# Kernel tuning notes

Hardware: AMD Instinct MI355X
Metric: run time of the kernel (lower is better)

## Reference

```python
import jax, jax.numpy as jnp
import numpy as np
from jax import lax

P = 3            # patch_size
H = W = 32       # spatial size forced by reshape to (32,32)
RATES = (1, 2, 4, 8)
DN = ('NCHW', 'OIHW', 'NCHW')


def setup_inputs() -> dict:
    key = jax.random.key(0)
    k0, k1, k2, k3 = jax.random.split(key, 4)
    foreground = jax.random.normal(k0, (8, 256, H, W), jnp.float32)
    background = jax.random.normal(k1, (8, 256, H, W), jnp.float32)
    mask = (jax.random.uniform(k2, (1, 1, H, W)) < 0.5).astype(jnp.float32)  # binary hole mask
    conv_w = jax.random.normal(k3, (4, 64, 256, 3, 3), jnp.float32) * 0.02
    conv_b = jnp.zeros((4, 64), jnp.float32)
    return {"foreground": foreground, "mask": mask, "background": background,
            "conv_w": conv_w, "conv_b": conv_b}


def _extract_patches(x):
    # x: [C, H+2, W+2] (padded) -> [H*W, C, 3, 3], patch index = h*W + w (torch unfold order)
    C = x.shape[0]
    cols = jnp.stack([x[:, i:i + H, j:j + W] for i in range(P) for j in range(P)], axis=0)  # [9,C,H,W]
    return cols.reshape(P, P, C, H, W).transpose(3, 4, 2, 0, 1).reshape(H * W, C, P, P)


def _forward(foreground, mask, background, conv_w, conv_b):
    bg = background * (1.0 - mask)
    bg_p = jnp.pad(bg, ((0, 0), (0, 0), (1, 1), (1, 1)))
    # per-sample patch kernels, L2-normalized (cosine similarity)
    kernels = jax.vmap(_extract_patches)(bg_p) + 1e-7          # [bz, L=1024, C, 3, 3]
    norm = jnp.sqrt(jnp.sum(kernels ** 2, axis=(2, 3, 4), keepdims=True))
    kernels = kernels / norm

    def corr(fm, kern):  # fm [C,H,W], kern [L,C,3,3] -> [L,H,W]
        return lax.conv_general_dilated(fm[None], kern, (1, 1), 'SAME', dimension_numbers=DN)[0]

    scores = jax.vmap(corr)(foreground, kernels)               # [bz, L, H, W]
    # propagation: depthwise 3x3 ones conv (groups=L, padding=1) == windowed sum
    scores = lax.reduce_window(scores, jnp.float32(0), lax.add,
                               (1, 1, 3, 3), (1, 1, 1, 1), 'SAME')
    attn = jax.nn.softmax(scores, axis=1)                      # softmax over the L patch axis

    def tconv(a, kern):
        # conv_transpose2d(a, kern[in=L,out=C], padding=1) == conv2d with spatially
        # flipped kernels and in/out swapped, padding = 3-1-1 = 1 (SAME)
        wct = jnp.flip(kern, axis=(2, 3)).transpose(1, 0, 2, 3)  # [C, L, 3, 3]
        return lax.conv_general_dilated(a[None], wct, (1, 1), 'SAME', dimension_numbers=DN)[0]

    recovered = jax.vmap(tconv)(attn, kernels)                 # [bz, C, H, W]
    recovered = recovered * mask / (P * P)
    final = recovered + foreground * (1.0 - mask)

    outs = []
    for g in range(4):  # 4 fused dilated conv branches (structurally distinct weights)
        r = RATES[g]
        o = lax.conv_general_dilated(final, conv_w[g], (1, 1), [(r, r), (r, r)],
                                     rhs_dilation=(r, r), dimension_numbers=DN)
        outs.append(jax.nn.relu(o + conv_b[g][None, :, None, None]))
    return jnp.concatenate(outs, axis=1)                       # [bz, 256, H, W]


def reference(foreground, mask, background, conv_w, conv_b):
    return _forward(foreground, mask, background, conv_w, conv_b)
```

## Files before the change

kernel.cpp:

```cpp
#include <hip/hip_runtime.h>

typedef __attribute__((ext_vector_type(8))) short short8;
typedef __attribute__((ext_vector_type(4))) float f32x4;
typedef __attribute__((ext_vector_type(4))) unsigned int uint4v;

#define HW 32
#define L 1024
#define C_IN 256
#define BATCH 8
#define NQ 1156

static __device__ __forceinline__ unsigned short f2bf(float f){
  unsigned int u = __float_as_uint(f);
  unsigned int r = (u + 0x7FFFu + ((u >> 16) & 1u)) >> 16;
  return (unsigned short)r;
}
static __device__ __forceinline__ float bf2f(unsigned short h){
  return __uint_as_float(((unsigned int)h) << 16);
}

#define GLDS16(g, l) __builtin_amdgcn_global_load_lds(                          \
    (const __attribute__((address_space(1))) void*)(g),                         \
    (__attribute__((address_space(3))) void*)(l), 16, 0, 0)

__global__ __launch_bounds__(256) void fused_prep(const float* __restrict__ fg,
                                                  const float* __restrict__ bgd,
                                                  const float* __restrict__ mask,
                                                  unsigned short* __restrict__ fgT,
                                                  unsigned short* __restrict__ mbgT,
                                                  unsigned short* __restrict__ mbgS,
                                                  float* __restrict__ psum,
                                                  const float* __restrict__ conv_w,
                                                  unsigned short* __restrict__ Wr,
                                                  unsigned short* __restrict__ zpage){
  __shared__ float T[64][65];
  int blk = blockIdx.x;
  if (blk >= 512){
    if (blk == 512) zpage[threadIdx.x] = 0;
    int idx = (blk - 512) * 256 + threadIdx.x;
    int c = idx & 255;
    int rest = idx >> 8;
    int n = rest & 63;
    int sg = rest >> 6;
    int s = sg % 9, g = sg / 9;
    Wr[idx] = f2bf(conv_w[(((size_t)(g * 64 + n)) * C_IN + c) * 9 + s]);
    return;
  }
  const int NP = BATCH * L;
  int bx = blk & 15, cb = (blk >> 4) & 3, b = blk >> 6;
  int p0 = bx * 64, c0 = cb * 64;
  int tid = threadIdx.x;
  int rr = tid >> 4, px = (tid & 15) * 4;
  int cx = tid & 15, ppb = tid >> 4;
  const float* F = fg  + ((size_t)b * C_IN + c0) * L + p0;
  const float* G = bgd + ((size_t)b * C_IN + c0) * L + p0;

  #pragma unroll
  for (int it = 0; it < 4; it++){
    int cc = it * 16 + rr;
    float4 v = *(const float4*)(F + (size_t)cc * L + px);
    T[cc][px] = v.x; T[cc][px + 1] = v.y; T[cc][px + 2] = v.z; T[cc][px + 3] = v.w;
  }
  __syncthreads();
  #pragma unroll
  for (int it = 0; it < 4; it++){
    int pp = it * 16 + ppb;
    float t0 = T[cx * 4][pp], t1 = T[cx * 4 + 1][pp], t2 = T[cx * 4 + 2][pp], t3 = T[cx * 4 + 3][pp];
    ushort4 o; o.x = f2bf(t0); o.y = f2bf(t1); o.z = f2bf(t2); o.w = f2bf(t3);
    *(ushort4*)&fgT[(size_t)(b * L + p0 + pp) * C_IN + c0 + cx * 4] = o;
    float s = t0 + t1 + t2 + t3;
    #pragma unroll
    for (int off = 8; off; off >>= 1) s += __shfl_xor(s, off, 16);
    if (cx == 0) psum[(size_t)(cb * 3 + 0) * NP + b * L + p0 + pp] = s;
  }
  __syncthreads();

  float4 mv = *(const float4*)(mask + p0 + px);
  mv.x = 1.f - mv.x; mv.y = 1.f - mv.y; mv.z = 1.f - mv.z; mv.w = 1.f - mv.w;
  #pragma unroll
  for (int it = 0; it < 4; it++){
    int cc = it * 16 + rr;
    float4 v = *(const float4*)(G + (size_t)cc * L + px);
    v.x *= mv.x; v.y *= mv.y; v.z *= mv.z; v.w *= mv.w;
    T[cc][px] = v.x; T[cc][px + 1] = v.y; T[cc][px + 2] = v.z; T[cc][px + 3] = v.w;
    ushort4 o; o.x = f2bf(v.x); o.y = f2bf(v.y); o.z = f2bf(v.z); o.w = f2bf(v.w);
    *(ushort4*)&mbgS[((size_t)b * C_IN + c0 + cc) * L + p0 + px] = o;
  }
  __syncthreads();
  #pragma unroll
  for (int it = 0; it < 4; it++){
    int pp = it * 16 + ppb;
    float t0 = T[cx * 4][pp], t1 = T[cx * 4 + 1][pp], t2 = T[cx * 4 + 2][pp], t3 = T[cx * 4 + 3][pp];
    ushort4 o; o.x = f2bf(t0); o.y = f2bf(t1); o.z = f2bf(t2); o.w = f2bf(t3);
    *(ushort4*)&mbgT[(size_t)(b * L + p0 + pp) * C_IN + c0 + cx * 4] = o;
    float s1 = t0 + t1 + t2 + t3;
    float s2 = t0 * t0 + t1 * t1 + t2 * t2 + t3 * t3;
    #pragma unroll
    for (int off = 8; off; off >>= 1){
      s1 += __shfl_xor(s1, off, 16);
      s2 += __shfl_xor(s2, off, 16);
    }
    if (cx == 0){
      psum[(size_t)(cb * 3 + 1) * NP + b * L + p0 + pp] = s1;
      psum[(size_t)(cb * 3 + 2) * NP + b * L + p0 + pp] = s2;
    }
  }
}

__global__ __launch_bounds__(256) void gemm_d_rn(const unsigned short* __restrict__ fgT,
                                                 const unsigned short* __restrict__ mbgT,
                                                 unsigned short* __restrict__ D,
                                                 const float* __restrict__ psum,
                                                 float* __restrict__ rn,
                                                 float* __restrict__ eps){
  __shared__ unsigned short As[64][256];
  __shared__ unsigned short Bs[64][256];
  int bid = blockIdx.x;
  if (bid >= 2048){
    int idx = (bid - 2048) * 256 + threadIdx.x;
    int b = idx >> 10, l = idx & 1023;
    int ly = l >> 5, lx = l & 31;
    const int NP = BATCH * L;
    float n2 = 2.304e-11f;
    #pragma unroll
    for (int s = 0; s < 9; s++){
      int y = ly + s / 3 - 1, x = lx + s % 3 - 1;
      if ((unsigned)y < HW && (unsigned)x < HW){
        int q = b * L + y * HW + x;
        float s1 = 0.f, s2 = 0.f;
        #pragma unroll
        for (int k = 0; k < 4; k++){
          s1 += psum[(size_t)(k * 3 + 1) * NP + q];
          s2 += psum[(size_t)(k * 3 + 2) * NP + q];
        }
        n2 += s2 + 2e-7f * s1;
      }
    }
    rn[idx] = 1.f / sqrtf(n2);
    float ev = 0.f;
    const int tw[5] = {1, 2, 3, 2, 1};
    #pragma unroll
    for (int oy = -2; oy <= 2; oy++)
      #pragma unroll
      for (int ox = -2; ox <= 2; ox++){
        int y = ly + oy, x = lx + ox;
        if ((unsigned)y < HW && (unsigned)x < HW){
          int q = b * L + y * HW + x;
          float s0 = 0.f;
          #pragma unroll
          for (int k = 0; k < 4; k++) s0 += psum[(size_t)(k * 3 + 0) * NP + q];
          ev += (float)(tw[oy + 2] * tw[ox + 2]) * s0;
        }
      }
    eps[idx] = 1e-7f * ev;
    return;
  }
  int b = bid & 7, r = bid >> 3;
  int by = r >> 4, bx = r & 15;
  const unsigned short* Ab = fgT  + ((size_t)b * L + by * 64) * C_IN;
  const unsigned short* Bb = mbgT + ((size_t)b * L + bx * 64) * C_IN;
  int tid = threadIdx.x, lane = tid & 63, wv = tid >> 6;
  int row_off = lane >> 5, slot = lane & 31;
  int q = slot >> 3, sl = slot & 7;
  #pragma unroll
  for (int i = 0; i < 8; i++){
    int rr = wv * 16 + i * 2 + row_off;
    int srcs = q * 8 + (sl ^ (rr & 7));
    GLDS16(Ab + (size_t)rr * C_IN + srcs * 8, &As[wv * 16 + i * 2][0]);
    GLDS16(Bb + (size_t)rr * C_IN + srcs * 8, &Bs[wv * 16 + i * 2][0]);
  }
  __syncthreads();
  int wm = (wv & 1) * 32, wn = (wv >> 1) * 32;
  int rsel = lane & 15, sx = lane >> 4;
  f32x4 acc[2][2] = {};
  #pragma unroll
  for (int st = 0; st < 8; st++){
    int gs = st * 4 + sx, qq = gs >> 3, ss = gs & 7;
    short8 af[2], bf[2];
    #pragma unroll
    for (int i = 0; i < 2; i++){
      int ra = wm + i * 16 + rsel;
      af[i] = *(const short8*)&As[ra][(qq * 8 + (ss ^ (ra & 7))) * 8];
      int rb = wn + i * 16 + rsel;
      bf[i] = *(const short8*)&Bs[rb][(qq * 8 + (ss ^ (rb & 7))) * 8];
    }
    #pragma unroll
    for (int i = 0; i < 2; i++)
      #pragma unroll
      for (int j = 0; j < 2; j++)
        acc[i][j] = __builtin_amdgcn_mfma_f32_16x16x32_bf16(af[i], bf[j], acc[i][j], 0, 0, 0);
  }
  unsigned short* Db = D + ((size_t)b << 20);
  int rowb = (lane >> 4) * 4, col = lane & 15;
  #pragma unroll
  for (int i = 0; i < 2; i++)
    #pragma unroll
    for (int j = 0; j < 2; j++)
      #pragma unroll
      for (int r2 = 0; r2 < 4; r2++)
        Db[(size_t)(by * 64 + wm + i * 16 + rowb + r2) * L + bx * 64 + wn + j * 16 + col] = f2bf(acc[i][j][r2]);
}

__global__ __launch_bounds__(256) void box3(const unsigned short* __restrict__ D,
                                            unsigned short* __restrict__ W){
  int bid = blockIdx.x;
  int b = bid & 7;
  int q2 = (bid >> 3) * 2 + (threadIdx.x >> 7);
  int v0 = (threadIdx.x & 127) * 8;
  int qy = q2 / 34 - 1, qx = q2 % 34 - 1;
  const unsigned short* Db = D + ((size_t)b << 20);
  float a[8] = {0.f, 0.f, 0.f, 0.f, 0.f, 0.f, 0.f, 0.f};
  #pragma unroll
  for (int dy = -1; dy <= 1; dy++)
    #pragma unroll
    for (int dx = -1; dx <= 1; dx++){
      int y = qy + dy, x = qx + dx;
      if ((unsigned)y < HW && (unsigned)x < HW){
        uint4v v = *(const uint4v*)(Db + ((size_t)(y * HW + x) << 10) + v0);
        #pragma unroll
        for (int j = 0; j < 4; j++){
          a[j * 2]     += __uint_as_float(v[j] << 16);
          a[j * 2 + 1] += __uint_as_float(v[j] & 0xffff0000u);
        }
      }
    }
  uint4v o;
  #pragma unroll
  for (int j = 0; j < 4; j++)
    o[j] = (unsigned)f2bf(a[j * 2]) | ((unsigned)f2bf(a[j * 2 + 1]) << 16);
  *(uint4v*)(W + ((size_t)(b * NQ + q2) << 10) + v0) = o;
}

static __device__ __forceinline__ void tap4(const unsigned* __restrict__ row32,
                                            int idx, int sh,
                                            unsigned &o0, unsigned &o1){
  int a0 = idx & ~3;
  const uint2* row = (const uint2*)row32;
  uint2 q0 = row[a0 >> 2];
  uint2 q1 = row[((a0 + 4) & 1023) >> 2];
  if (sh == 0){ o0 = q0.x; o1 = q0.y; }
  else if (sh == 1){ o0 = (q0.x >> 16) | (q0.y << 16); o1 = (q0.y >> 16) | (q1.x << 16); }
  else if (sh == 2){ o0 = q0.y; o1 = q1.x; }
  else { o0 = (q0.y >> 16) | (q1.x << 16); o1 = (q1.x >> 16) | (q1.y << 16); }
}

__global__ __launch_bounds__(256) void prop_softmax_diag(const unsigned short* __restrict__ W,
                                                         const float* __restrict__ eps,
                                                         const float* __restrict__ rn,
                                                         unsigned short* __restrict__ AR){
  __shared__ __align__(16) unsigned short Wl[16][1024];
  __shared__ float redm[4][4], reds[4][4];
  int bid = blockIdx.x;
  int b = bid & 7, tile = bid >> 3;
  int py0 = (tile >> 4) * 2, px0 = (tile & 15) * 2;
  const unsigned short* Wb = W + (size_t)b * NQ * L;
  int tid = threadIdx.x, lane = tid & 63, wv = tid >> 6;
  #pragma unroll
  for (int k = 0; k < 8; k++){
    int u = k * 4 + wv;
    int rr = u >> 1, half = u & 1;
    int qs = (py0 + (rr >> 2)) * 34 + (px0 + (rr & 3));
    GLDS16(Wb + (((size_t)qs) << 10) + half * 512 + lane * 8, &Wl[rr][half * 512]);
  }
  int l0 = tid * 4;
  int ly = l0 >> 5, lx0 = l0 & 31;
  float4 rnl = *(const float4*)&rn[b * L + l0];
  float ev[4];
  #pragma unroll
  for (int o = 0; o < 4; o++)
    ev[o] = eps[b * L + (py0 + (o >> 1)) * HW + (px0 + (o & 1))];
  __syncthreads();
  float val[4][4];
  #pragma unroll
  for (int o = 0; o < 4; o++){
    int oy = o >> 1, ox = o & 1;
    float a[4] = {0.f, 0.f, 0.f, 0.f};
    #pragma unroll
    for (int s = 0; s < 9; s++){
      const int dy = s / 3 - 1, dx = s % 3 - 1;
      const int dlt = dy * 32 + dx;
      const int sh = dlt & 3;
      bool rok = (unsigned)(ly + dy) < HW;
      int idx = (l0 + dlt) & 1023;
      unsigned o0, o1;
      tap4((const unsigned*)&Wl[(oy + dy + 1) * 4 + (ox + dx + 1)][0], idx, sh, o0, o1);
      float f0 = __uint_as_float(o0 << 16), f1 = __uint_as_float(o0 & 0xffff0000u);
      float f2 = __uint_as_float(o1 << 16), f3 = __uint_as_float(o1 & 0xffff0000u);
      a[0] += (rok && (unsigned)(lx0 + 0 + dx) < HW) ? f0 : 0.f;
      a[1] += (rok && (unsigned)(lx0 + 1 + dx) < HW) ? f1 : 0.f;
      a[2] += (rok && (unsigned)(lx0 + 2 + dx) < HW) ? f2 : 0.f;
      a[3] += (rok && (unsigned)(lx0 + 3 + dx) < HW) ? f3 : 0.f;
    }
    val[o][0] = rnl.x * (a[0] + ev[o]); val[o][1] = rnl.y * (a[1] + ev[o]);
    val[o][2] = rnl.z * (a[2] + ev[o]); val[o][3] = rnl.w * (a[3] + ev[o]);
  }
  #pragma unroll
  for (int o = 0; o < 4; o++){
    float m = fmaxf(fmaxf(val[o][0], val[o][1]), fmaxf(val[o][2], val[o][3]));
    #pragma unroll
    for (int off = 32; off; off >>= 1) m = fmaxf(m, __shfl_xor(m, off));
    if (lane == 0) redm[wv][o] = m;
  }
  __syncthreads();
  float mf[4];
  #pragma unroll
  for (int o = 0; o < 4; o++)
    mf[o] = fmaxf(fmaxf(redm[0][o], redm[1][o]), fmaxf(redm[2][o], redm[3][o]));
  float e[4][4];
  #pragma unroll
  for (int o = 0; o < 4; o++){
    float t = 0.f;
    #pragma unroll
    for (int j = 0; j < 4; j++){ e[o][j] = __expf(val[o][j] - mf[o]); t += e[o][j]; }
    #pragma unroll
    for (int off = 32; off; off >>= 1) t += __shfl_xor(t, off);
    if (lane == 0) reds[wv][o] = t;
  }
  __syncthreads();
  #pragma unroll
  for (int o = 0; o < 4; o++){
    float inv = 1.f / (reds[0][o] + reds[1][o] + reds[2][o] + reds[3][o]);
    int p = (py0 + (o >> 1)) * HW + (px0 + (o & 1));
    unsigned short* O = AR + ((size_t)b << 20) + ((size_t)p << 10);
    ushort4 ov;
    ov.x = f2bf(e[o][0] * inv * rnl.x); ov.y = f2bf(e[o][1] * inv * rnl.y);
    ov.z = f2bf(e[o][2] * inv * rnl.z); ov.w = f2bf(e[o][3] * inv * rnl.w);
    *(ushort4*)&O[l0] = ov;
  }
}

__global__ __launch_bounds__(256) void u_stencil(const unsigned short* __restrict__ AR,
                                                 unsigned short* __restrict__ U){
  __shared__ __align__(16) unsigned short Al[16][1024];
  int bid = blockIdx.x;
  int b = bid & 7, tile = bid >> 3;
  int py0 = (tile >> 4) * 2, px0 = (tile & 15) * 2;
  int tid = threadIdx.x, lane = tid & 63, wv = tid >> 6;
  const unsigned short* A = AR + ((size_t)b << 20);
  #pragma unroll
  for (int k = 0; k < 8; k++){
    int u = k * 4 + wv;
    int rr = u >> 1, half = u & 1;
    int yy = py0 + (rr >> 2) - 1, xx = px0 + (rr & 3) - 1;
    bool rok = ((unsigned)yy < HW) && ((unsigned)xx < HW);
    int p2 = rok ? (yy * HW + xx) : 0;
    GLDS16(A + (((size_t)p2) << 10) + half * 512 + lane * 8, &Al[rr][half * 512]);
  }
  int vmask = 0;
  #pragma unroll
  for (int rr = 0; rr < 16; rr++){
    int yy = py0 + (rr >> 2) - 1, xx = px0 + (rr & 3) - 1;
    if (((unsigned)yy < HW) && ((unsigned)xx < HW)) vmask |= 1 << rr;
  }
  __syncthreads();
  int v0 = tid * 4;
  int vy = v0 >> 5, vx0 = v0 & 31;
  #pragma unroll
  for (int o = 0; o < 4; o++){
    int oy = o >> 1, ox = o & 1;
    float acc[4] = {0.f, 0.f, 0.f, 0.f};
    #pragma unroll
    for (int s = 0; s < 9; s++){
      const int dy = s / 3 - 1, dx = s % 3 - 1;
      const int dlt = dy * 32 + dx;
      const int sh = dlt & 3;
      const int rr = (oy + dy + 1) * 4 + (ox + dx + 1);
      bool rok = ((vmask >> rr) & 1) && ((unsigned)(vy + dy) < HW);
      int idx = (v0 + dlt) & 1023;
      unsigned o0, o1;
      tap4((const unsigned*)&Al[rr][0], idx, sh, o0, o1);
      float f0 = __uint_as_float(o0 << 16), f1 = __uint_as_float(o0 & 0xffff0000u);
      float f2 = __uint_as_float(o1 << 16), f3 = __uint_as_float(o1 & 0xffff0000u);
      acc[0] += (rok && (unsigned)(vx0 + 0 + dx) < HW) ? f0 : 0.f;
      acc[1] += (rok && (unsigned)(vx0 + 1 + dx) < HW) ? f1 : 0.f;
      acc[2] += (rok && (unsigned)(vx0 + 2 + dx) < HW) ? f2 : 0.f;
      acc[3] += (rok && (unsigned)(vx0 + 3 + dx) < HW) ? f3 : 0.f;
    }
    int p = (py0 + oy) * HW + (px0 + ox);
    unsigned short* O = U + ((size_t)b << 20) + ((size_t)p << 10);
    ushort4 ov;
    ov.x = f2bf(acc[0]); ov.y = f2bf(acc[1]); ov.z = f2bf(acc[2]); ov.w = f2bf(acc[3]);
    *(ushort4*)&O[v0] = ov;
  }
}

__global__ __launch_bounds__(256) void gemm3_final(const unsigned short* __restrict__ U,
                                                   const unsigned short* __restrict__ mbgS,
                                                   const float* __restrict__ mask,
                                                   const unsigned short* __restrict__ fgT,
                                                   unsigned short* __restrict__ finalT){
  __shared__ unsigned short As[2][64][64];
  __shared__ unsigned short Bs[2][64][64];
  int bid = blockIdx.x;
  int b = bid & 7, r = bid >> 3;
  int mt = r >> 2, ct = r & 3;
  int tid = threadIdx.x, lane = tid & 63, wv = tid >> 6;
  int wm = (wv & 1) * 32, wn = (wv >> 1) * 32;
  int rsel = lane & 15;
  int srow = lane >> 3, scol = ((lane & 7) ^ srow) * 8;
  const unsigned short* Ab = U    + ((size_t)b * L + mt * 64) * L;
  const unsigned short* Bb = mbgS + ((size_t)b * C_IN + ct * 64) * L;
  #pragma unroll
  for (int g8 = 0; g8 < 2; g8++){
    GLDS16(Ab + (size_t)(wv * 16 + g8 * 8 + srow) * L + scol, &As[0][wv * 16 + g8 * 8][0]);
    GLDS16(Bb + (size_t)(wv * 16 + g8 * 8 + srow) * L + scol, &Bs[0][wv * 16 + g8 * 8][0]);
  }
  __syncthreads();
  f32x4 acc[2][2] = {};
  int cur = 0;
  for (int t = 0; t < 16; ++t){
    short8 af[2][2], bf[2][2];
    #pragma unroll
    for (int kk = 0; kk < 2; kk++){
      int s0 = kk * 4 + (lane >> 4);
      int col = ((s0 ^ (rsel & 7)) << 3);
      #pragma unroll
      for (int i = 0; i < 2; i++){
        af[kk][i] = *(const short8*)&As[cur][wm + i * 16 + rsel][col];
        bf[kk][i] = *(const short8*)&Bs[cur][wn + i * 16 + rsel][col];
      }
    }
    if (t + 1 < 16){
      int nb = cur ^ 1;
      size_t kt = (size_t)(t + 1) * 64;
      #pragma unroll
      for (int g8 = 0; g8 < 2; g8++){
        GLDS16(Ab + (size_t)(wv * 16 + g8 * 8 + srow) * L + kt + scol, &As[nb][wv * 16 + g8 * 8][0]);
        GLDS16(Bb + (size_t)(wv * 16 + g8 * 8 + srow) * L + kt + scol, &Bs[nb][wv * 16 + g8 * 8][0]);
      }
    }
    #pragma unroll
    for (int kk = 0; kk < 2; kk++)
      #pragma unroll
      for (int i = 0; i < 2; i++)
        #pragma unroll
        for (int j = 0; j < 2; j++)
          acc[i][j] = __builtin_amdgcn_mfma_f32_16x16x32_bf16(af[kk][i], bf[kk][j], acc[i][j], 0, 0, 0);
    __syncthreads();
    cur ^= 1;
  }
  int rowb = (lane >> 4) * 4, col = lane & 15;
  #pragma unroll
  for (int i = 0; i < 2; i++)
    #pragma unroll
    for (int j = 0; j < 2; j++)
      #pragma unroll
      for (int r2 = 0; r2 < 4; r2++){
        int p = mt * 64 + wm + i * 16 + rowb + r2;
        int c = ct * 64 + wn + j * 16 + col;
        unsigned short o;
        if (mask[p] != 0.f) o = f2bf(acc[i][j][r2] * (1.f / 9.f));
        else                o = fgT[((size_t)b * L + p) * C_IN + c];
        finalT[((size_t)b * L + p) * C_IN + c] = o;
      }
}

__global__ __launch_bounds__(256) void branch_gemm(const unsigned short* __restrict__ finalT,
                                                   const unsigned short* __restrict__ Wr,
                                                   const float* __restrict__ conv_b,
                                                   const unsigned short* __restrict__ zpage,
                                                   float* __restrict__ out){
  __shared__ unsigned short As[2][64][64];
  __shared__ unsigned short Bs[2][64][64];
  int nwg = gridDim.x, bid = blockIdx.x;
  int nid = (bid & 7) * (nwg >> 3) + (bid >> 3);
  int bg = nid >> 4, pt = nid & 15;
  int b = bg >> 2, g = bg & 3;
  int rate = 1 << g;
  int p0 = pt * 64;
  int tid = threadIdx.x, lane = tid & 63, wv = tid >> 6;
  int wm = (wv & 1) * 32, wn = (wv >> 1) * 32;
  int rsel = lane & 15;
  int srow = lane >> 3;
  int scol = ((lane & 7) ^ srow) * 8;
  const unsigned short* FT = finalT + (size_t)b * L * C_IN;
  const unsigned short* WG = Wr + (size_t)(g * 9) * 64 * C_IN;

  int ay[2], ax[2];
  #pragma unroll
  for (int g8 = 0; g8 < 2; g8++){
    int p = p0 + wv * 16 + g8 * 8 + srow;
    ay[g8] = p >> 5; ax[g8] = p & 31;
  }
  auto a_src = [&](int t, int g8) -> const unsigned short* {
    int s = t >> 2, q = t & 3;
    int dy = s / 3 - 1, dx = s - (s / 3) * 3 - 1;
    int iy = ay[g8] + rate * dy, ix = ax[g8] + rate * dx;
    if ((unsigned)iy < HW && (unsigned)ix < HW)
      return FT + (size_t)(iy * HW + ix) * C_IN + q * 64 + scol;
    return zpage;
  };
  auto b_src = [&](int t, int g8) -> const unsigned short* {
    int s = t >> 2, q = t & 3;
    int n = wv * 16 + g8 * 8 + srow;
    return WG + (size_t)(s * 64 + n) * C_IN + q * 64 + scol;
  };

  f32x4 acc[2][2] = {};
  #pragma unroll
  for (int g8 = 0; g8 < 2; g8++){
    GLDS16(a_src(0, g8), &As[0][wv * 16 + g8 * 8][0]);
    GLDS16(b_src(0, g8), &Bs[0][wv * 16 + g8 * 8][0]);
  }
  __syncthreads();
  int cur = 0;
  for (int t = 0; t < 36; ++t){
    short8 af[2][2], bf[2][2];
    #pragma unroll
    for (int kk = 0; kk < 2; kk++){
      int s0 = kk * 4 + (lane >> 4);
      int col = ((s0 ^ (rsel & 7)) << 3);
      #pragma unroll
      for (int i = 0; i < 2; i++){
        af[kk][i] = *(const short8*)&As[cur][wm + i * 16 + rsel][col];
        bf[kk][i] = *(const short8*)&Bs[cur][wn + i * 16 + rsel][col];
      }
    }
    if (t + 1 < 36){
      int nb = cur ^ 1;
      #pragma unroll
      for (int g8 = 0; g8 < 2; g8++){
        GLDS16(a_src(t + 1, g8), &As[nb][wv * 16 + g8 * 8][0]);
        GLDS16(b_src(t + 1, g8), &Bs[nb][wv * 16 + g8 * 8][0]);
      }
    }
    #pragma unroll
    for (int kk = 0; kk < 2; kk++)
      #pragma unroll
      for (int i = 0; i < 2; i++)
        #pragma unroll
        for (int j = 0; j < 2; j++)
          acc[i][j] = __builtin_amdgcn_mfma_f32_16x16x32_bf16(af[kk][i], bf[kk][j], acc[i][j], 0, 0, 0);
    __syncthreads();
    cur ^= 1;
  }
  int rowb = (lane >> 4) * 4, col = lane & 15;
  float* O = out + (size_t)(b * 256 + g * 64) * L;
  #pragma unroll
  for (int i = 0; i < 2; i++)
    #pragma unroll
    for (int j = 0; j < 2; j++){
      int n = wn + j * 16 + col;
      float bias = conv_b[g * 64 + n];
      #pragma unroll
      for (int r2 = 0; r2 < 4; r2++){
        int p = p0 + wm + i * 16 + rowb + r2;
        O[(size_t)n * L + p] = fmaxf(acc[i][j][r2] + bias, 0.f);
      }
    }
}


extern "C" void kernel_launch(void* const* d_in, const int* in_sizes, int n_in,
                              void* d_out, int out_size, void* d_ws, size_t ws_size,
                              hipStream_t stream){
  const float* fg     = (const float*)d_in[0];
  const float* mask   = (const float*)d_in[1];
  const float* bgd    = (const float*)d_in[2];
  const float* conv_w = (const float*)d_in[3];
  const float* conv_b = (const float*)d_in[4];

  char* ws = (char*)d_ws;
  unsigned short* D      = (unsigned short*)(ws + 0);
  unsigned short* W      = (unsigned short*)(ws + 16777216);
  unsigned short* AR     = (unsigned short*)(ws + 35717120);
  unsigned short* U      = (unsigned short*)(ws + 52494336);
  unsigned short* mbgT   = (unsigned short*)(ws + 69271552);
  unsigned short* mbgS   = (unsigned short*)(ws + 73465856);
  unsigned short* finalT = (unsigned short*)(ws + 77660160);
  unsigned short* Wr     = (unsigned short*)(ws + 81854464);
  float*          psum   = (float*)(ws + 83034112);
  float*          rn     = (float*)(ws + 83427328);
  float*          eps    = (float*)(ws + 83460096);
  unsigned short* zpage  = (unsigned short*)(ws + 83492864);
  unsigned short* fgT    = (unsigned short*)d_out;
  float* out = (float*)d_out;

  fused_prep<<<2816, 256, 0, stream>>>(fg, bgd, mask, fgT, mbgT, mbgS, psum,
                                       conv_w, Wr, zpage);
  gemm_d_rn<<<2080, 256, 0, stream>>>(fgT, mbgT, D, psum, rn, eps);
  box3<<<4624, 256, 0, stream>>>(D, W);
  prop_softmax_diag<<<2048, 256, 0, stream>>>(W, eps, rn, AR);
  u_stencil<<<2048, 256, 0, stream>>>(AR, U);
  gemm3_final<<<512, 256, 0, stream>>>(U, mbgS, mask, fgT, finalT);
  branch_gemm<<<512, 256, 0, stream>>>(finalT, Wr, conv_b, zpage, out);
}
```

Measured before the change: 108.8 us.

## Double block size to 512 threads across GEMM and stencil kernels

```diff
diff --git a/kernel.cpp b/kernel.cpp
--- a/kernel.cpp
+++ b/kernel.cpp
@@ -107,7 +107,7 @@
   }
 }
 
-__global__ __launch_bounds__(256) void gemm_d_rn(const unsigned short* __restrict__ fgT,
+__global__ __launch_bounds__(512) void gemm_d_rn(const unsigned short* __restrict__ fgT,
                                                  const unsigned short* __restrict__ mbgT,
                                                  unsigned short* __restrict__ D,
                                                  const float* __restrict__ psum,
@@ -117,7 +117,7 @@
   __shared__ unsigned short Bs[64][256];
   int bid = blockIdx.x;
   if (bid >= 2048){
-    int idx = (bid - 2048) * 256 + threadIdx.x;
+    int idx = (bid - 2048) * 512 + threadIdx.x;
     int b = idx >> 10, l = idx & 1023;
     int ly = l >> 5, lx = l & 31;
     const int NP = BATCH * L;
@@ -163,42 +163,38 @@
   int row_off = lane >> 5, slot = lane & 31;
   int q = slot >> 3, sl = slot & 7;
   #pragma unroll
-  for (int i = 0; i < 8; i++){
-    int rr = wv * 16 + i * 2 + row_off;
+  for (int i = 0; i < 4; i++){
+    int rr = wv * 8 + i * 2 + row_off;
     int srcs = q * 8 + (sl ^ (rr & 7));
-    GLDS16(Ab + (size_t)rr * C_IN + srcs * 8, &As[wv * 16 + i * 2][0]);
-    GLDS16(Bb + (size_t)rr * C_IN + srcs * 8, &Bs[wv * 16 + i * 2][0]);
-  }
-  __syncthreads();
-  int wm = (wv & 1) * 32, wn = (wv >> 1) * 32;
+    GLDS16(Ab + (size_t)rr * C_IN + srcs * 8, &As[wv * 8 + i * 2][0]);
+    GLDS16(Bb + (size_t)rr * C_IN + srcs * 8, &Bs[wv * 8 + i * 2][0]);
+  }
+  __syncthreads();
+  int wm = (wv & 1) * 32, wn = (wv >> 1) * 16;
   int rsel = lane & 15, sx = lane >> 4;
-  f32x4 acc[2][2] = {};
+  f32x4 acc[2] = {};
   #pragma unroll
   for (int st = 0; st < 8; st++){
     int gs = st * 4 + sx, qq = gs >> 3, ss = gs & 7;
-    short8 af[2], bf[2];
+    short8 af[2], bf;
     #pragma unroll
     for (int i = 0; i < 2; i++){
       int ra = wm + i * 16 + rsel;
       af[i] = *(const short8*)&As[ra][(qq * 8 + (ss ^ (ra & 7))) * 8];
-      int rb = wn + i * 16 + rsel;
-      bf[i] = *(const short8*)&Bs[rb][(qq * 8 + (ss ^ (rb & 7))) * 8];
-    }
+    }
+    int rb = wn + rsel;
+    bf = *(const short8*)&Bs[rb][(qq * 8 + (ss ^ (rb & 7))) * 8];
     #pragma unroll
     for (int i = 0; i < 2; i++)
-      #pragma unroll
-      for (int j = 0; j < 2; j++)
-        acc[i][j] = __builtin_amdgcn_mfma_f32_16x16x32_bf16(af[i], bf[j], acc[i][j], 0, 0, 0);
+      acc[i] = __builtin_amdgcn_mfma_f32_16x16x32_bf16(af[i], bf, acc[i], 0, 0, 0);
   }
   unsigned short* Db = D + ((size_t)b << 20);
   int rowb = (lane >> 4) * 4, col = lane & 15;
   #pragma unroll
   for (int i = 0; i < 2; i++)
     #pragma unroll
-    for (int j = 0; j < 2; j++)
-      #pragma unroll
-      for (int r2 = 0; r2 < 4; r2++)
-        Db[(size_t)(by * 64 + wm + i * 16 + rowb + r2) * L + bx * 64 + wn + j * 16 + col] = f2bf(acc[i][j][r2]);
+    for (int r2 = 0; r2 < 4; r2++)
+      Db[(size_t)(by * 64 + wm + i * 16 + rowb + r2) * L + bx * 64 + wn + col] = f2bf(acc[i][r2]);
 }
 
 __global__ __launch_bounds__(256) void box3(const unsigned short* __restrict__ D,
@@ -231,72 +227,63 @@
   *(uint4v*)(W + ((size_t)(b * NQ + q2) << 10) + v0) = o;
 }
 
-static __device__ __forceinline__ void tap4(const unsigned* __restrict__ row32,
-                                            int idx, int sh,
-                                            unsigned &o0, unsigned &o1){
-  int a0 = idx & ~3;
-  const uint2* row = (const uint2*)row32;
-  uint2 q0 = row[a0 >> 2];
-  uint2 q1 = row[((a0 + 4) & 1023) >> 2];
-  if (sh == 0){ o0 = q0.x; o1 = q0.y; }
-  else if (sh == 1){ o0 = (q0.x >> 16) | (q0.y << 16); o1 = (q0.y >> 16) | (q1.x << 16); }
-  else if (sh == 2){ o0 = q0.y; o1 = q1.x; }
-  else { o0 = (q0.y >> 16) | (q1.x << 16); o1 = (q1.x >> 16) | (q1.y << 16); }
-}
-
-__global__ __launch_bounds__(256) void prop_softmax_diag(const unsigned short* __restrict__ W,
+static __device__ __forceinline__ unsigned tap2(const unsigned* __restrict__ row32,
+                                                int idx, int sh){
+  int a0 = idx & ~1;
+  unsigned q0 = row32[a0 >> 1];
+  if (sh == 0) return q0;
+  unsigned q1 = row32[((a0 + 2) & 1023) >> 1];
+  return (q0 >> 16) | (q1 << 16);
+}
+
+__global__ __launch_bounds__(512) void prop_softmax_diag(const unsigned short* __restrict__ W,
                                                          const float* __restrict__ eps,
                                                          const float* __restrict__ rn,
                                                          unsigned short* __restrict__ AR){
   __shared__ __align__(16) unsigned short Wl[16][1024];
-  __shared__ float redm[4][4], reds[4][4];
+  __shared__ float redm[8][4], reds[8][4];
   int bid = blockIdx.x;
   int b = bid & 7, tile = bid >> 3;
   int py0 = (tile >> 4) * 2, px0 = (tile & 15) * 2;
   const unsigned short* Wb = W + (size_t)b * NQ * L;
   int tid = threadIdx.x, lane = tid & 63, wv = tid >> 6;
   #pragma unroll
-  for (int k = 0; k < 8; k++){
-    int u = k * 4 + wv;
+  for (int k = 0; k < 4; k++){
+    int u = k * 8 + wv;
     int rr = u >> 1, half = u & 1;
     int qs = (py0 + (rr >> 2)) * 34 + (px0 + (rr & 3));
     GLDS16(Wb + (((size_t)qs) << 10) + half * 512 + lane * 8, &Wl[rr][half * 512]);
   }
-  int l0 = tid * 4;
+  int l0 = tid * 2;
   int ly = l0 >> 5, lx0 = l0 & 31;
-  float4 rnl = *(const float4*)&rn[b * L + l0];
+  float2 rnl = *(const float2*)&rn[b * L + l0];
   float ev[4];
   #pragma unroll
   for (int o = 0; o < 4; o++)
     ev[o] = eps[b * L + (py0 + (o >> 1)) * HW + (px0 + (o & 1))];
   __syncthreads();
-  float val[4][4];
+  float val[4][2];
   #pragma unroll
   for (int o = 0; o < 4; o++){
     int oy = o >> 1, ox = o & 1;
-    float a[4] = {0.f, 0.f, 0.f, 0.f};
+    float a0 = 0.f, a1 = 0.f;
     #pragma unroll
     for (int s = 0; s < 9; s++){
       const int dy = s / 3 - 1, dx = s % 3 - 1;
       const int dlt = dy * 32 + dx;
-      const int sh = dlt & 3;
+      const int sh = dx & 1;
       bool rok = (unsigned)(ly + dy) < HW;
       int idx = (l0 + dlt) & 1023;
-      unsigned o0, o1;
-      tap4((const unsigned*)&Wl[(oy + dy + 1) * 4 + (ox + dx + 1)][0], idx, sh, o0, o1);
-      float f0 = __uint_as_float(o0 << 16), f1 = __uint_as_float(o0 & 0xffff0000u);
-      float f2 = __uint_as_float(o1 << 16), f3 = __uint_as_float(o1 & 0xffff0000u);
-      a[0] += (rok && (unsigned)(lx0 + 0 + dx) < HW) ? f0 : 0.f;
-      a[1] += (rok && (unsigned)(lx0 + 1 + dx) < HW) ? f1 : 0.f;
-      a[2] += (rok && (unsigned)(lx0 + 2 + dx) < HW) ? f2 : 0.f;
-      a[3] += (rok && (unsigned)(lx0 + 3 + dx) < HW) ? f3 : 0.f;
-    }
-    val[o][0] = rnl.x * (a[0] + ev[o]); val[o][1] = rnl.y * (a[1] + ev[o]);
-    val[o][2] = rnl.z * (a[2] + ev[o]); val[o][3] = rnl.w * (a[3] + ev[o]);
+      unsigned ov = tap2((const unsigned*)&Wl[(oy + dy + 1) * 4 + (ox + dx + 1)][0], idx, sh);
+      float f0 = __uint_as_float(ov << 16), f1 = __uint_as_float(ov & 0xffff0000u);
+      a0 += (rok && (unsigned)(lx0 + 0 + dx) < HW) ? f0 : 0.f;
+      a1 += (rok && (unsigned)(lx0 + 1 + dx) < HW) ? f1 : 0.f;
+    }
+    val[o][0] = rnl.x * (a0 + ev[o]); val[o][1] = rnl.y * (a1 + ev[o]);
   }
   #pragma unroll
   for (int o = 0; o < 4; o++){
-    float m = fmaxf(fmaxf(val[o][0], val[o][1]), fmaxf(val[o][2], val[o][3]));
+    float m = fmaxf(val[o][0], val[o][1]);
     #pragma unroll
     for (int off = 32; off; off >>= 1) m = fmaxf(m, __shfl_xor(m, off));
     if (lane == 0) redm[wv][o] = m;
@@ -304,14 +291,18 @@
   __syncthreads();
   float mf[4];
   #pragma unroll
-  for (int o = 0; o < 4; o++)
-    mf[o] = fmaxf(fmaxf(redm[0][o], redm[1][o]), fmaxf(redm[2][o], redm[3][o]));
-  float e[4][4];
-  #pragma unroll
   for (int o = 0; o < 4; o++){
-    float t = 0.f;
-    #pragma unroll
-    for (int j = 0; j < 4; j++){ e[o][j] = __expf(val[o][j] - mf[o]); t += e[o][j]; }
+    float m = redm[0][o];
+    #pragma unroll
+    for (int w = 1; w < 8; w++) m = fmaxf(m, redm[w][o]);
+    mf[o] = m;
+  }
+  float e[4][2];
+  #pragma unroll
+  for (int o = 0; o < 4; o++){
+    e[o][0] = __expf(val[o][0] - mf[o]);
+    e[o][1] = __expf(val[o][1] - mf[o]);
+    float t = e[o][0] + e[o][1];
     #pragma unroll
     for (int off = 32; off; off >>= 1) t += __shfl_xor(t, off);
     if (lane == 0) reds[wv][o] = t;
@@ -319,17 +310,19 @@
   __syncthreads();
   #pragma unroll
   for (int o = 0; o < 4; o++){
-    float inv = 1.f / (reds[0][o] + reds[1][o] + reds[2][o] + reds[3][o]);
+    float t = reds[0][o];
+    #pragma unroll
+    for (int w = 1; w < 8; w++) t += reds[w][o];
+    float inv = 1.f / t;
     int p = (py0 + (o >> 1)) * HW + (px0 + (o & 1));
     unsigned short* O = AR + ((size_t)b << 20) + ((size_t)p << 10);
-    ushort4 ov;
+    ushort2 ov;
     ov.x = f2bf(e[o][0] * inv * rnl.x); ov.y = f2bf(e[o][1] * inv * rnl.y);
-    ov.z = f2bf(e[o][2] * inv * rnl.z); ov.w = f2bf(e[o][3] * inv * rnl.w);
-    *(ushort4*)&O[l0] = ov;
-  }
-}
-
-__global__ __launch_bounds__(256) void u_stencil(const unsigned short* __restrict__ AR,
+    *(ushort2*)&O[l0] = ov;
+  }
+}
+
+__global__ __launch_bounds__(512) void u_stencil(const unsigned short* __restrict__ AR,
                                                  unsigned short* __restrict__ U){
   __shared__ __align__(16) unsigned short Al[16][1024];
   int bid = blockIdx.x;
@@ -338,8 +331,8 @@
   int tid = threadIdx.x, lane = tid & 63, wv = tid >> 6;
   const unsigned short* A = AR + ((size_t)b << 20);
   #pragma unroll
-  for (int k = 0; k < 8; k++){
-    int u = k * 4 + wv;
+  for (int k = 0; k < 4; k++){
+    int u = k * 8 + wv;
     int rr = u >> 1, half = u & 1;
     int yy = py0 + (rr >> 2) - 1, xx = px0 + (rr & 3) - 1;
     bool rok = ((unsigned)yy < HW) && ((unsigned)xx < HW);
@@ -353,38 +346,34 @@
     if (((unsigned)yy < HW) && ((unsigned)xx < HW)) vmask |= 1 << rr;
   }
   __syncthreads();
-  int v0 = tid * 4;
+  int v0 = tid * 2;
   int vy = v0 >> 5, vx0 = v0 & 31;
   #pragma unroll
   for (int o = 0; o < 4; o++){
     int oy = o >> 1, ox = o & 1;
-    float acc[4] = {0.f, 0.f, 0.f, 0.f};
+    float a0 = 0.f, a1 = 0.f;
     #pragma unroll
     for (int s = 0; s < 9; s++){
       const int dy = s / 3 - 1, dx = s % 3 - 1;
       const int dlt = dy * 32 + dx;
-      const int sh = dlt & 3;
+      const int sh = dx & 1;
       const int rr = (oy + dy + 1) * 4 + (ox + dx + 1);
       bool rok = ((vmask >> rr) & 1) && ((unsigned)(vy + dy) < HW);
       int idx = (v0 + dlt) & 1023;
-      unsigned o0, o1;
-      tap4((const unsigned*)&Al[rr][0], idx, sh, o0, o1);
-      float f0 = __uint_as_float(o0 << 16), f1 = __uint_as_float(o0 & 0xffff0000u);
-      float f2 = __uint_as_float(o1 << 16), f3 = __uint_as_float(o1 & 0xffff0000u);
-      acc[0] += (rok && (unsigned)(vx0 + 0 + dx) < HW) ? f0 : 0.f;
-      acc[1] += (rok && (unsigned)(vx0 + 1 + dx) < HW) ? f1 : 0.f;
-      acc[2] += (rok && (unsigned)(vx0 + 2 + dx) < HW) ? f2 : 0.f;
-      acc[3] += (rok && (unsigned)(vx0 + 3 + dx) < HW) ? f3 : 0.f;
+      unsigned ov = tap2((const unsigned*)&Al[rr][0], idx, sh);
+      float f0 = __uint_as_float(ov << 16), f1 = __uint_as_float(ov & 0xffff0000u);
+      a0 += (rok && (unsigned)(vx0 + 0 + dx) < HW) ? f0 : 0.f;
+      a1 += (rok && (unsigned)(vx0 + 1 + dx) < HW) ? f1 : 0.f;
     }
     int p = (py0 + oy) * HW + (px0 + ox);
     unsigned short* O = U + ((size_t)b << 20) + ((size_t)p << 10);
-    ushort4 ov;
-    ov.x = f2bf(acc[0]); ov.y = f2bf(acc[1]); ov.z = f2bf(acc[2]); ov.w = f2bf(acc[3]);
-    *(ushort4*)&O[v0] = ov;
-  }
-}
-
-__global__ __launch_bounds__(256) void gemm3_final(const unsigned short* __restrict__ U,
+    ushort2 ov2;
+    ov2.x = f2bf(a0); ov2.y = f2bf(a1);
+    *(ushort2*)&O[v0] = ov2;
+  }
+}
+
+__global__ __launch_bounds__(512) void gemm3_final(const unsigned short* __restrict__ U,
                                                    const unsigned short* __restrict__ mbgS,
                                                    const float* __restrict__ mask,
                                                    const unsigned short* __restrict__ fgT,
@@ -395,47 +384,38 @@
   int b = bid & 7, r = bid >> 3;
   int mt = r >> 2, ct = r & 3;
   int tid = threadIdx.x, lane = tid & 63, wv = tid >> 6;
-  int wm = (wv & 1) * 32, wn = (wv >> 1) * 32;
+  int wm = (wv & 1) * 32, wn = (wv >> 1) * 16;
   int rsel = lane & 15;
   int srow = lane >> 3, scol = ((lane & 7) ^ srow) * 8;
   const unsigned short* Ab = U    + ((size_t)b * L + mt * 64) * L;
   const unsigned short* Bb = mbgS + ((size_t)b * C_IN + ct * 64) * L;
-  #pragma unroll
-  for (int g8 = 0; g8 < 2; g8++){
-    GLDS16(Ab + (size_t)(wv * 16 + g8 * 8 + srow) * L + scol, &As[0][wv * 16 + g8 * 8][0]);
-    GLDS16(Bb + (size_t)(wv * 16 + g8 * 8 + srow) * L + scol, &Bs[0][wv * 16 + g8 * 8][0]);
-  }
-  __syncthreads();
-  f32x4 acc[2][2] = {};
+  GLDS16(Ab + (size_t)(wv * 8 + srow) * L + scol, &As[0][wv * 8][0]);
+  GLDS16(Bb + (size_t)(wv * 8 + srow) * L + scol, &Bs[0][wv * 8][0]);
+  __syncthreads();
+  f32x4 acc[2] = {};
   int cur = 0;
   for (int t = 0; t < 16; ++t){
-    short8 af[2][2], bf[2][2];
+    short8 af[2][2], bf[2];
     #pragma unroll
     for (int kk = 0; kk < 2; kk++){
       int s0 = kk * 4 + (lane >> 4);
       int col = ((s0 ^ (rsel & 7)) << 3);
       #pragma unroll
-      for (int i = 0; i < 2; i++){
+      for (int i = 0; i < 2; i++)
         af[kk][i] = *(const short8*)&As[cur][wm + i * 16 + rsel][col];
-        bf[kk][i] = *(const short8*)&Bs[cur][wn + i * 16 + rsel][col];
-      }
+      bf[kk] = *(const short8*)&Bs[cur][wn + rsel][col];
     }
     if (t + 1 < 16){
       int nb = cur ^ 1;
       size_t kt = (size_t)(t + 1) * 64;
-      #pragma unroll
-      for (int g8 = 0; g8 < 2; g8++){
-        GLDS16(Ab + (size_t)(wv * 16 + g8 * 8 + srow) * L + kt + scol, &As[nb][wv * 16 + g8 * 8][0]);
-        GLDS16(Bb + (size_t)(wv * 16 + g8 * 8 + srow) * L + kt + scol, &Bs[nb][wv * 16 + g8 * 8][0]);
-      }
+      GLDS16(Ab + (size_t)(wv * 8 + srow) * L + kt + scol, &As[nb][wv * 8][0]);
+      GLDS16(Bb + (size_t)(wv * 8 + srow) * L + kt + scol, &Bs[nb][wv * 8][0]);
     }
     #pragma unroll
     for (int kk = 0; kk < 2; kk++)
       #pragma unroll
       for (int i = 0; i < 2; i++)
-        #pragma unroll
-        for (int j = 0; j < 2; j++)
-          acc[i][j] = __builtin_amdgcn_mfma_f32_16x16x32_bf16(af[kk][i], bf[kk][j], acc[i][j], 0, 0, 0);
+        acc[i] = __builtin_amdgcn_mfma_f32_16x16x32_bf16(af[kk][i], bf[kk], acc[i], 0, 0, 0);
     __syncthreads();
     cur ^= 1;
   }
@@ -443,19 +423,17 @@
   #pragma unroll
   for (int i = 0; i < 2; i++)
     #pragma unroll
-    for (int j = 0; j < 2; j++)
-      #pragma unroll
-      for (int r2 = 0; r2 < 4; r2++){
-        int p = mt * 64 + wm + i * 16 + rowb + r2;
-        int c = ct * 64 + wn + j * 16 + col;
-        unsigned short o;
-        if (mask[p] != 0.f) o = f2bf(acc[i][j][r2] * (1.f / 9.f));
-        else                o = fgT[((size_t)b * L + p) * C_IN + c];
-        finalT[((size_t)b * L + p) * C_IN + c] = o;
-      }
-}
-
-__global__ __launch_bounds__(256) void branch_gemm(const unsigned short* __restrict__ finalT,
+    for (int r2 = 0; r2 < 4; r2++){
+      int p = mt * 64 + wm + i * 16 + rowb + r2;
+      int c = ct * 64 + wn + col;
+      unsigned short o;
+      if (mask[p] != 0.f) o = f2bf(acc[i][r2] * (1.f / 9.f));
+      else                o = fgT[((size_t)b * L + p) * C_IN + c];
+      finalT[((size_t)b * L + p) * C_IN + c] = o;
+    }
+}
+
+__global__ __launch_bounds__(512) void branch_gemm(const unsigned short* __restrict__ finalT,
                                                    const unsigned short* __restrict__ Wr,
                                                    const float* __restrict__ conv_b,
                                                    const unsigned short* __restrict__ zpage,
@@ -469,84 +447,68 @@
   int rate = 1 << g;
   int p0 = pt * 64;
   int tid = threadIdx.x, lane = tid & 63, wv = tid >> 6;
-  int wm = (wv & 1) * 32, wn = (wv >> 1) * 32;
+  int wm = (wv & 1) * 32, wn = (wv >> 1) * 16;
   int rsel = lane & 15;
   int srow = lane >> 3;
   int scol = ((lane & 7) ^ srow) * 8;
   const unsigned short* FT = finalT + (size_t)b * L * C_IN;
   const unsigned short* WG = Wr + (size_t)(g * 9) * 64 * C_IN;
 
-  int ay[2], ax[2];
-  #pragma unroll
-  for (int g8 = 0; g8 < 2; g8++){
-    int p = p0 + wv * 16 + g8 * 8 + srow;
-    ay[g8] = p >> 5; ax[g8] = p & 31;
-  }
-  auto a_src = [&](int t, int g8) -> const unsigned short* {
+  int prow = p0 + wv * 8 + srow;
+  int ayy = prow >> 5, axx = prow & 31;
+  auto a_src = [&](int t) -> const unsigned short* {
     int s = t >> 2, q = t & 3;
     int dy = s / 3 - 1, dx = s - (s / 3) * 3 - 1;
-    int iy = ay[g8] + rate * dy, ix = ax[g8] + rate * dx;
+    int iy = ayy + rate * dy, ix = axx + rate * dx;
     if ((unsigned)iy < HW && (unsigned)ix < HW)
       return FT + (size_t)(iy * HW + ix) * C_IN + q * 64 + scol;
     return zpage;
   };
-  auto b_src = [&](int t, int g8) -> const unsigned short* {
+  auto b_src = [&](int t) -> const unsigned short* {
     int s = t >> 2, q = t & 3;
-    int n = wv * 16 + g8 * 8 + srow;
+    int n = wv * 8 + srow;
     return WG + (size_t)(s * 64 + n) * C_IN + q * 64 + scol;
   };
 
-  f32x4 acc[2][2] = {};
-  #pragma unroll
-  for (int g8 = 0; g8 < 2; g8++){
-    GLDS16(a_src(0, g8), &As[0][wv * 16 + g8 * 8][0]);
-    GLDS16(b_src(0, g8), &Bs[0][wv * 16 + g8 * 8][0]);
-  }
+  f32x4 acc[2] = {};
+  GLDS16(a_src(0), &As[0][wv * 8][0]);
+  GLDS16(b_src(0), &Bs[0][wv * 8][0]);
   __syncthreads();
   int cur = 0;
   for (int t = 0; t < 36; ++t){
-    short8 af[2][2], bf[2][2];
+    short8 af[2][2], bf[2];
     #pragma unroll
     for (int kk = 0; kk < 2; kk++){
       int s0 = kk * 4 + (lane >> 4);
       int col = ((s0 ^ (rsel & 7)) << 3);
       #pragma unroll
-      for (int i = 0; i < 2; i++){
+      for (int i = 0; i < 2; i++)
         af[kk][i] = *(const short8*)&As[cur][wm + i * 16 + rsel][col];
-        bf[kk][i] = *(const short8*)&Bs[cur][wn + i * 16 + rsel][col];
-      }
+      bf[kk] = *(const short8*)&Bs[cur][wn + rsel][col];
     }
     if (t + 1 < 36){
       int nb = cur ^ 1;
-      #pragma unroll
-      for (int g8 = 0; g8 < 2; g8++){
-        GLDS16(a_src(t + 1, g8), &As[nb][wv * 16 + g8 * 8][0]);
-        GLDS16(b_src(t + 1, g8), &Bs[nb][wv * 16 + g8 * 8][0]);
-      }
+      GLDS16(a_src(t + 1), &As[nb][wv * 8][0]);
+      GLDS16(b_src(t + 1), &Bs[nb][wv * 8][0]);
     }
     #pragma unroll
     for (int kk = 0; kk < 2; kk++)
       #pragma unroll
       for (int i = 0; i < 2; i++)
-        #pragma unroll
-        for (int j = 0; j < 2; j++)
-          acc[i][j] = __builtin_amdgcn_mfma_f32_16x16x32_bf16(af[kk][i], bf[kk][j], acc[i][j], 0, 0, 0);
+        acc[i] = __builtin_amdgcn_mfma_f32_16x16x32_bf16(af[kk][i], bf[kk], acc[i], 0, 0, 0);
     __syncthreads();
     cur ^= 1;
   }
   int rowb = (lane >> 4) * 4, col = lane & 15;
   float* O = out + (size_t)(b * 256 + g * 64) * L;
+  int n = wn + col;
+  float bias = conv_b[g * 64 + n];
   #pragma unroll
   for (int i = 0; i < 2; i++)
     #pragma unroll
-    for (int j = 0; j < 2; j++){
-      int n = wn + j * 16 + col;
-      float bias = conv_b[g * 64 + n];
-      #pragma unroll
-      for (int r2 = 0; r2 < 4; r2++){
-        int p = p0 + wm + i * 16 + rowb + r2;
-        O[(size_t)n * L + p] = fmaxf(acc[i][j][r2] + bias, 0.f);
-      }
+    for (int r2 = 0; r2 < 4; r2++){
+      int p = p0 + wm + i * 16 + rowb + r2;
+      O[(size_t)n * L + p] = fmaxf(acc[i][r2] + bias, 0.f);
     }
 }
 
@@ -578,10 +540,10 @@
 
   fused_prep<<<2816, 256, 0, stream>>>(fg, bgd, mask, fgT, mbgT, mbgS, psum,
                                        conv_w, Wr, zpage);
-  gemm_d_rn<<<2080, 256, 0, stream>>>(fgT, mbgT, D, psum, rn, eps);
+  gemm_d_rn<<<2064, 512, 0, stream>>>(fgT, mbgT, D, psum, rn, eps);
   box3<<<4624, 256, 0, stream>>>(D, W);
-  prop_softmax_diag<<<2048, 256, 0, stream>>>(W, eps, rn, AR);
-  u_stencil<<<2048, 256, 0, stream>>>(AR, U);
-  gemm3_final<<<512, 256, 0, stream>>>(U, mbgS, mask, fgT, finalT);
-  branch_gemm<<<512, 256, 0, stream>>>(finalT, Wr, conv_b, zpage, out);
-}
+  prop_softmax_diag<<<2048, 512, 0, stream>>>(W, eps, rn, AR);
+  u_stencil<<<2048, 512, 0, stream>>>(AR, U);
+  gemm3_final<<<512, 512, 0, stream>>>(U, mbgS, mask, fgT, finalT);
+  branch_gemm<<<512, 512, 0, stream>>>(finalT, Wr, conv_b, zpage, out);
+}
```

New measurement: 108.8 us. No clear change (+0.1%).
